# Optimization experiments

Hardware: AMD Instinct MI355X
Metric: run time of the kernel (lower is better)

Reference implementation:

```python
import jax, jax.numpy as jnp
import numpy as np

N = 50000   # nodes
E = 600000  # edges
HID = 128   # node_hidden_channels
G = 128     # num_edge_gaussians
C = 128     # num_node_interaction_channels
EPS = 1e-5  # batchnorm eps


def setup_inputs() -> dict:
    key = jax.random.key(0)
    ks = jax.random.split(key, 12)
    s = lambda k, shape, fan_in: jax.random.normal(k, shape, jnp.float32) / np.sqrt(fan_in)
    return {
        "h": jax.random.normal(ks[0], (N, HID), jnp.float32),
        "edge_index": jax.random.randint(ks[1], (2, E), 0, N),
        "edge_weight": jax.random.uniform(ks[2], (E,), jnp.float32),
        "edge_attr": jax.random.normal(ks[3], (E, G), jnp.float32),
        # lin0: HID -> C
        "W0": s(ks[4], (HID, C), HID), "b0": jnp.zeros((C,), jnp.float32),
        # short: G -> 1
        "Wsh": s(ks[5], (G, 1), G), "bsh": jnp.zeros((1,), jnp.float32),
        # CGConv lin_f / lin_s: (2C+1) -> C, rows ordered [x_i; x_j; edge_attr]
        "Wf": s(ks[6], (2 * C + 1, C), 2 * C + 1), "bf": jnp.zeros((C,), jnp.float32),
        "Ws": s(ks[7], (2 * C + 1, C), 2 * C + 1), "bs": jnp.zeros((C,), jnp.float32),
        # BatchNorm1d affine params
        "gamma": jnp.ones((C,), jnp.float32), "beta": jnp.zeros((C,), jnp.float32),
    }


def reference(h, edge_index, edge_weight, edge_attr, W0, b0, Wsh, bsh, Wf, bf, Ws, bs, gamma, beta):
    src = edge_index[0]  # j (source)
    dst = edge_index[1]  # i (target / aggregation index)

    out = jax.nn.softplus(h @ W0 + b0)                    # [N, C]
    e = jax.nn.softplus(edge_attr @ Wsh + bsh)            # [E, 1]

    # CGConv: z = [x_i, x_j, e]; msg = sigmoid(lin_f(z)) * softplus(lin_s(z))
    # Split the linears so node parts are computed once per node, not per edge.
    pi_f = out @ Wf[:C]          # x_i part  [N, C]
    pj_f = out @ Wf[C:2 * C]     # x_j part  [N, C]
    pi_s = out @ Ws[:C]
    pj_s = out @ Ws[C:2 * C]
    ef = e @ Wf[2 * C:]          # edge part [E, C]
    es = e @ Ws[2 * C:]

    gate = jax.nn.sigmoid(pi_f[dst] + pj_f[src] + ef + bf)   # [E, C]
    core = jax.nn.softplus(pi_s[dst] + pj_s[src] + es + bs)  # [E, C]
    aggr = jax.ops.segment_sum(gate * core, dst, num_segments=N)  # [N, C]

    # BatchNorm1d (training-mode batch statistics) + residual inside CGConv
    mean = jnp.mean(aggr, axis=0)
    var = jnp.var(aggr, axis=0)
    bn = (aggr - mean) * jax.lax.rsqrt(var + EPS) * gamma + beta
    conv_out = bn + out

    # _Interactions: out = out + conv(out)
    return out + conv_out
```

## Files before the change

### kernel.cpp

```cpp
#include <hip/hip_runtime.h>
#include <cmath>

#define NN 50000
#define EE 600000

#define LOG2E 1.44269504088896340736f
#define LN2F  0.69314718055994530942f

__device__ __forceinline__ float fast_exp2(float x) { return __builtin_amdgcn_exp2f(x); }
__device__ __forceinline__ float fast_log2(float x) { return __builtin_amdgcn_logf(x); }
__device__ __forceinline__ float fast_rcp(float x)  { return __builtin_amdgcn_rcpf(x); }

__device__ __forceinline__ float softplus_fast(float x) {
  float x2 = x * LOG2E;
  return LN2F * (fmaxf(x2, 0.f) + fast_log2(1.f + fast_exp2(-fabsf(x2))));
}

__global__ __launch_bounds__(256) void zero_kernel(int* __restrict__ deg,
                                                   float* __restrict__ stats_f) {
  int i = blockIdx.x * 256 + threadIdx.x;
  if (i < NN) deg[i] = 0;
  if (i < 512) stats_f[i] = 0.f;
}

__global__ __launch_bounds__(256) void gemm128_act(const float* __restrict__ A,
                                                   const float* __restrict__ B,
                                                   const float* __restrict__ bias,
                                                   float* __restrict__ Cmat,
                                                   int nrows) {
  __shared__ float Ash[64][68];
  __shared__ float Bsh[64][128];
  const int tid = threadIdx.x;
  const int row0 = blockIdx.x * 64;
  const int tx = tid & 15, ty = tid >> 4;
  const int r0 = ty * 4, c0 = tx * 4;

  float acc[4][8];
#pragma unroll
  for (int r = 0; r < 4; ++r)
#pragma unroll
    for (int j = 0; j < 8; ++j) acc[r][j] = 0.f;

  for (int kb = 0; kb < 2; ++kb) {
    for (int i = tid; i < 64 * 16; i += 256) {
      int r = i >> 4, k4 = i & 15;
      int gr = row0 + r; if (gr >= nrows) gr = nrows - 1;
      float4 v = ((const float4*)(A + (size_t)gr * 128 + kb * 64))[k4];
      *(float4*)&Ash[r][k4 * 4] = v;
    }
    for (int i = tid; i < 64 * 32; i += 256) {
      int k = i >> 5, c4 = i & 31;
      float4 v = ((const float4*)(B + (size_t)(kb * 64 + k) * 128))[c4];
      *(float4*)&Bsh[k][c4 * 4] = v;
    }
    __syncthreads();
#pragma unroll 4
    for (int k = 0; k < 64; ++k) {
      float aa[4] = {Ash[r0 + 0][k], Ash[r0 + 1][k], Ash[r0 + 2][k], Ash[r0 + 3][k]};
      float4 b0 = *(const float4*)&Bsh[k][c0];
      float4 b1 = *(const float4*)&Bsh[k][c0 + 64];
      float bb[8] = {b0.x, b0.y, b0.z, b0.w, b1.x, b1.y, b1.z, b1.w};
#pragma unroll
      for (int r = 0; r < 4; ++r)
#pragma unroll
        for (int j = 0; j < 8; ++j) acc[r][j] = fmaf(aa[r], bb[j], acc[r][j]);
    }
    __syncthreads();
  }

  float bv[8];
#pragma unroll
  for (int j = 0; j < 8; ++j) bv[j] = bias[j < 4 ? c0 + j : c0 + 60 + j];
#pragma unroll
  for (int r = 0; r < 4; ++r) {
    int gr = row0 + r0 + r;
    if (gr < nrows) {
      float tmp[8];
#pragma unroll
      for (int j = 0; j < 8; ++j) tmp[j] = softplus_fast(acc[r][j] + bv[j]);
      *(float4*)(Cmat + (size_t)gr * 128 + c0) = make_float4(tmp[0], tmp[1], tmp[2], tmp[3]);
      *(float4*)(Cmat + (size_t)gr * 128 + c0 + 64) = make_float4(tmp[4], tmp[5], tmp[6], tmp[7]);
    }
  }
}

__global__ __launch_bounds__(256) void gemm128_p4(const float* __restrict__ A,
                                                  const float* __restrict__ Wf,
                                                  const float* __restrict__ Ws,
                                                  const float* __restrict__ bf,
                                                  const float* __restrict__ bs,
                                                  float* __restrict__ Pif,
                                                  float* __restrict__ Pjf,
                                                  float* __restrict__ Pis,
                                                  float* __restrict__ Pjs,
                                                  int nrows) {
  __shared__ float Ash[64][68];
  __shared__ float Bsh[64][128];
  const int tid = threadIdx.x;
  const int row0 = blockIdx.x * 64;
  const int which = blockIdx.y;

  const float* B;  const float* bias;  float* Cmat;
  if (which == 0)      { B = Wf;             bias = bf;      Cmat = Pif; }
  else if (which == 1) { B = Wf + 128 * 128; bias = nullptr; Cmat = Pjf; }
  else if (which == 2) { B = Ws;             bias = bs;      Cmat = Pis; }
  else                 { B = Ws + 128 * 128; bias = nullptr; Cmat = Pjs; }

  const int tx = tid & 15, ty = tid >> 4;
  const int r0 = ty * 4, c0 = tx * 4;

  float acc[4][8];
#pragma unroll
  for (int r = 0; r < 4; ++r)
#pragma unroll
    for (int j = 0; j < 8; ++j) acc[r][j] = 0.f;

  for (int kb = 0; kb < 2; ++kb) {
    for (int i = tid; i < 64 * 16; i += 256) {
      int r = i >> 4, k4 = i & 15;
      int gr = row0 + r; if (gr >= nrows) gr = nrows - 1;
      float4 v = ((const float4*)(A + (size_t)gr * 128 + kb * 64))[k4];
      *(float4*)&Ash[r][k4 * 4] = v;
    }
    for (int i = tid; i < 64 * 32; i += 256) {
      int k = i >> 5, c4 = i & 31;
      float4 v = ((const float4*)(B + (size_t)(kb * 64 + k) * 128))[c4];
      *(float4*)&Bsh[k][c4 * 4] = v;
    }
    __syncthreads();
#pragma unroll 4
    for (int k = 0; k < 64; ++k) {
      float aa[4] = {Ash[r0 + 0][k], Ash[r0 + 1][k], Ash[r0 + 2][k], Ash[r0 + 3][k]};
      float4 b0 = *(const float4*)&Bsh[k][c0];
      float4 b1 = *(const float4*)&Bsh[k][c0 + 64];
      float bb[8] = {b0.x, b0.y, b0.z, b0.w, b1.x, b1.y, b1.z, b1.w};
#pragma unroll
      for (int r = 0; r < 4; ++r)
#pragma unroll
        for (int j = 0; j < 8; ++j) acc[r][j] = fmaf(aa[r], bb[j], acc[r][j]);
    }
    __syncthreads();
  }

  float bv[8];
#pragma unroll
  for (int j = 0; j < 8; ++j)
    bv[j] = bias ? bias[j < 4 ? c0 + j : c0 + 60 + j] : 0.f;
#pragma unroll
  for (int r = 0; r < 4; ++r) {
    int gr = row0 + r0 + r;
    if (gr < nrows) {
      float tmp[8];
#pragma unroll
      for (int j = 0; j < 8; ++j) tmp[j] = (acc[r][j] + bv[j]) * LOG2E;
      *(float4*)(Cmat + (size_t)gr * 128 + c0) = make_float4(tmp[0], tmp[1], tmp[2], tmp[3]);
      *(float4*)(Cmat + (size_t)gr * 128 + c0 + 64) = make_float4(tmp[4], tmp[5], tmp[6], tmp[7]);
    }
  }
}

__global__ __launch_bounds__(256) void edge_e_kernel(const float* __restrict__ edge_attr,
                                                     const float* __restrict__ Wsh,
                                                     const float* __restrict__ bsh,
                                                     float* __restrict__ ebuf) {
  __shared__ float wsh[128];
  int tid = threadIdx.x;
  if (tid < 128) wsh[tid] = Wsh[tid];
  __syncthreads();
  int wave = tid >> 6, lane = tid & 63;
  int sub = lane >> 4, l16 = lane & 15;
  int edge = (blockIdx.x * 4 + wave) * 4 + sub;
  const float4* row = (const float4*)(edge_attr + (size_t)edge * 128);
  float4 v0 = row[l16], v1 = row[l16 + 16];
  float4 w0 = *(const float4*)&wsh[l16 * 4];
  float4 w1 = *(const float4*)&wsh[64 + l16 * 4];
  float p = v0.x * w0.x + v0.y * w0.y + v0.z * w0.z + v0.w * w0.w +
            v1.x * w1.x + v1.y * w1.y + v1.z * w1.z + v1.w * w1.w;
  p += __shfl_xor(p, 1);
  p += __shfl_xor(p, 2);
  p += __shfl_xor(p, 4);
  p += __shfl_xor(p, 8);
  if (l16 == 0) ebuf[edge] = softplus_fast(p + bsh[0]);
}

__global__ __launch_bounds__(256) void hist_kernel(const int* __restrict__ eidx,
                                                   int* __restrict__ deg) {
  int e = blockIdx.x * 256 + threadIdx.x;
  if (e < EE) atomicAdd(&deg[eidx[EE + e]], 1);
}

__global__ __launch_bounds__(1024) void scan_kernel(const int* __restrict__ deg,
                                                    int* __restrict__ rowptr,
                                                    int* __restrict__ cur) {
  __shared__ int wscan[16];
  __shared__ int chunk_total_sh;
  int tid = threadIdx.x;
  int wid = tid >> 6, lane = tid & 63;
  int running = 0;
  for (int base = 0; base < NN; base += 4096) {
    int i0 = base + tid * 4;
    int4 v = make_int4(0, 0, 0, 0);
    if (i0 + 3 < NN) {
      v = *(const int4*)(deg + i0);
    } else {
      if (i0 < NN)     v.x = deg[i0];
      if (i0 + 1 < NN) v.y = deg[i0 + 1];
      if (i0 + 2 < NN) v.z = deg[i0 + 2];
      if (i0 + 3 < NN) v.w = deg[i0 + 3];
    }
    int t0 = v.x, t1 = t0 + v.y, t2 = t1 + v.z, t3 = t2 + v.w;
    int s = t3;
#pragma unroll
    for (int off = 1; off < 64; off <<= 1) {
      int t = __shfl_up(s, off);
      if (lane >= off) s += t;
    }
    if (lane == 63) wscan[wid] = s;
    __syncthreads();
    if (wid == 0 && lane < 16) {
      int w = wscan[lane];
#pragma unroll
      for (int off = 1; off < 16; off <<= 1) {
        int t = __shfl_up(w, off);
        if (lane >= off) w += t;
      }
      wscan[lane] = w;
      if (lane == 15) chunk_total_sh = w;
    }
    __syncthreads();
    int wexcl = (wid == 0) ? 0 : wscan[wid - 1];
    int texcl = running + wexcl + (s - t3);
    int4 r = make_int4(texcl, texcl + t0, texcl + t1, texcl + t2);
    if (i0 + 3 < NN) {
      *(int4*)(rowptr + i0) = r;
      *(int4*)(cur + i0) = r;
    } else {
      if (i0 < NN)     { rowptr[i0] = r.x;     cur[i0] = r.x; }
      if (i0 + 1 < NN) { rowptr[i0 + 1] = r.y; cur[i0 + 1] = r.y; }
      if (i0 + 2 < NN) { rowptr[i0 + 2] = r.z; cur[i0 + 2] = r.z; }
      if (i0 + 3 < NN) { rowptr[i0 + 3] = r.w; cur[i0 + 3] = r.w; }
    }
    running += chunk_total_sh;
    __syncthreads();
  }
  if (tid == 0) rowptr[NN] = EE;
}

__global__ __launch_bounds__(256) void scatter_kernel(const int* __restrict__ eidx,
                                                      const float* __restrict__ ebuf,
                                                      int* __restrict__ cur,
                                                      int* __restrict__ srcs,
                                                      float* __restrict__ evals) {
  int e = blockIdx.x * 256 + threadIdx.x;
  if (e < EE) {
    int dst = eidx[EE + e];
    int pos = atomicAdd(&cur[dst], 1);
    srcs[pos] = eidx[e];
    evals[pos] = ebuf[e];
  }
}

__global__ __launch_bounds__(256) void aggregate_kernel(const int* __restrict__ rowptr,
                                                        const int* __restrict__ srcs,
                                                        const float* __restrict__ evals,
                                                        float* __restrict__ pifagg,
                                                        const float* __restrict__ Pjf,
                                                        const float* __restrict__ Pis,
                                                        const float* __restrict__ Pjs,
                                                        const float* __restrict__ Wf_e,
                                                        const float* __restrict__ Ws_e) {
  __shared__ float wfe[128], wse[128];
  int tid = threadIdx.x;
  if (tid < 128) wfe[tid] = Wf_e[tid] * LOG2E;
  else wse[tid - 128] = Ws_e[tid - 128] * LOG2E;
  __syncthreads();
  int slot = tid >> 5, lane = tid & 31;
  int node = blockIdx.x * 8 + slot;
  float4 fi = ((const float4*)(pifagg + (size_t)node * 128))[lane];
  float4 si = ((const float4*)(Pis + (size_t)node * 128))[lane];
  float4 wf4 = *(const float4*)&wfe[lane * 4];
  float4 ws4 = *(const float4*)&wse[lane * 4];
  float4 acc = make_float4(0.f, 0.f, 0.f, 0.f);

  int beg = rowptr[node], end = rowptr[node + 1];
  if (beg < end) {
    int src = srcs[beg];
    float eV = evals[beg];
    float4 fj = ((const float4*)(Pjf + (size_t)src * 128))[lane];
    float4 sj = ((const float4*)(Pjs + (size_t)src * 128))[lane];
    int sN = 0; float eN = 0.f;
    if (beg + 1 < end) { sN = srcs[beg + 1]; eN = evals[beg + 1]; }
    for (int k = beg; ; ) {
      bool more = (k + 1 < end);
      float4 fjn, sjn;
      if (more) {
        fjn = ((const float4*)(Pjf + (size_t)sN * 128))[lane];
        sjn = ((const float4*)(Pjs + (size_t)sN * 128))[lane];
      }
      int sNN = 0; float eNN = 0.f;
      if (k + 2 < end) { sNN = srcs[k + 2]; eNN = evals[k + 2]; }
      {
        float a2, b2, g, sp;
        a2 = fmaf(eV, wf4.x, fi.x) + fj.x;
        g  = fast_rcp(1.f + fast_exp2(-a2));
        b2 = fmaf(eV, ws4.x, si.x) + sj.x;
        sp = fmaxf(b2, 0.f) + fast_log2(1.f + fast_exp2(-fabsf(b2)));
        acc.x = fmaf(g, sp, acc.x);
        a2 = fmaf(eV, wf4.y, fi.y) + fj.y;
        g  = fast_rcp(1.f + fast_exp2(-a2));
        b2 = fmaf(eV, ws4.y, si.y) + sj.y;
        sp = fmaxf(b2, 0.f) + fast_log2(1.f + fast_exp2(-fabsf(b2)));
        acc.y = fmaf(g, sp, acc.y);
        a2 = fmaf(eV, wf4.z, fi.z) + fj.z;
        g  = fast_rcp(1.f + fast_exp2(-a2));
        b2 = fmaf(eV, ws4.z, si.z) + sj.z;
        sp = fmaxf(b2, 0.f) + fast_log2(1.f + fast_exp2(-fabsf(b2)));
        acc.z = fmaf(g, sp, acc.z);
        a2 = fmaf(eV, wf4.w, fi.w) + fj.w;
        g  = fast_rcp(1.f + fast_exp2(-a2));
        b2 = fmaf(eV, ws4.w, si.w) + sj.w;
        sp = fmaxf(b2, 0.f) + fast_log2(1.f + fast_exp2(-fabsf(b2)));
        acc.w = fmaf(g, sp, acc.w);
      }
      if (!more) break;
      fj = fjn; sj = sjn; eV = eN; sN = sNN; eN = eNN; ++k;
    }
  }
  acc.x *= LN2F; acc.y *= LN2F; acc.z *= LN2F; acc.w *= LN2F;
  ((float4*)(pifagg + (size_t)node * 128))[lane] = acc;
}

__global__ __launch_bounds__(256) void stats_kernel(const float* __restrict__ aggr,
                                                    double* __restrict__ dstats) {
  int tid = threadIdx.x;
  int c = tid & 127, half = tid >> 7;
  int rbase = blockIdx.x * 512;
  float s = 0.f, q = 0.f;
  for (int i = 0; i < 256; ++i) {
    int r = rbase + half + i * 2;
    if (r < NN) {
      float v = aggr[(size_t)r * 128 + c];
      s += v;
      q += v * v;
    }
  }
  __shared__ float shs[256], shq[256];
  shs[tid] = s;
  shq[tid] = q;
  __syncthreads();
  if (tid < 128) {
    double ts = (double)shs[tid] + (double)shs[tid + 128];
    double tq = (double)shq[tid] + (double)shq[tid + 128];
    atomicAdd(&dstats[c], ts);
    atomicAdd(&dstats[128 + c], tq);
  }
}

__global__ void bn_params_kernel(const double* __restrict__ dstats,
                                 const float* __restrict__ gamma,
                                 const float* __restrict__ beta,
                                 float* __restrict__ scsh) {
  int c = threadIdx.x;
  double mean = dstats[c] / (double)NN;
  double var = dstats[128 + c] / (double)NN - mean * mean;
  double rs = 1.0 / sqrt(var + 1e-5);
  double sc = (double)gamma[c] * rs;
  scsh[c] = (float)sc;
  scsh[128 + c] = (float)((double)beta[c] - mean * sc);
}

__global__ __launch_bounds__(256) void finalize_kernel(const float* __restrict__ outbuf,
                                                       const float* __restrict__ scsh,
                                                       float* __restrict__ dout) {
  __shared__ float sc[128], sh[128];
  int tid = threadIdx.x;
  if (tid < 128) sc[tid] = scsh[tid];
  else sh[tid - 128] = scsh[tid];
  __syncthreads();
  size_t i = (size_t)blockIdx.x * 256 + tid;
  size_t stride = (size_t)gridDim.x * 256;
  const float4* o4 = (const float4*)outbuf;
  float4* d4 = (float4*)dout;
  const size_t n4 = (size_t)NN * 32;
  for (; i < n4; i += stride) {
    int c4 = (int)(i & 31) * 4;
    float4 a = d4[i], o = o4[i];
    float4 r;
    r.x = 2.f * o.x + a.x * sc[c4 + 0] + sh[c4 + 0];
    r.y = 2.f * o.y + a.y * sc[c4 + 1] + sh[c4 + 1];
    r.z = 2.f * o.z + a.z * sc[c4 + 2] + sh[c4 + 2];
    r.w = 2.f * o.w + a.w * sc[c4 + 3] + sh[c4 + 3];
    d4[i] = r;
  }
}

extern "C" void kernel_launch(void* const* d_in, const int* in_sizes, int n_in,
                              void* d_out, int out_size, void* d_ws, size_t ws_size,
                              hipStream_t stream) {
  const float* h         = (const float*)d_in[0];
  const int*   eidx      = (const int*)d_in[1];
  const float* edge_attr = (const float*)d_in[3];
  const float* W0    = (const float*)d_in[4];
  const float* b0    = (const float*)d_in[5];
  const float* Wsh   = (const float*)d_in[6];
  const float* bsh   = (const float*)d_in[7];
  const float* Wf    = (const float*)d_in[8];
  const float* bf    = (const float*)d_in[9];
  const float* Ws    = (const float*)d_in[10];
  const float* bs    = (const float*)d_in[11];
  const float* gamma = (const float*)d_in[12];
  const float* beta  = (const float*)d_in[13];
  float* dout = (float*)d_out;

  char* ws = (char*)d_ws;
  const size_t NCb = (size_t)NN * 128 * 4;
  float*  outbuf = (float*)ws;
  float*  Pjf    = (float*)(ws + NCb);
  float*  Pis    = (float*)(ws + NCb * 2);
  float*  Pjs    = (float*)(ws + NCb * 3);
  char*   p0     = ws + NCb * 4;
  float*  ebuf   = (float*)p0;                  p0 += (size_t)EE * 4;
  int*    srcs   = (int*)p0;                    p0 += (size_t)EE * 4;
  float*  evals  = (float*)p0;                  p0 += (size_t)EE * 4;
  double* dstats = (double*)p0;                 p0 += 256 * 8;
  float*  scsh   = (float*)p0;                  p0 += 256 * 4;
  int*    deg    = (int*)p0;                    p0 += (size_t)NN * 4;
  int*    rowptr = (int*)p0;                    p0 += (size_t)(NN + 4) * 4;
  int*    cur    = (int*)p0;
  float*  Pif    = dout;

  zero_kernel<<<(NN + 255) / 256, 256, 0, stream>>>(deg, (float*)dstats);

  const int gblocks = (NN + 63) / 64;
  gemm128_act<<<gblocks, 256, 0, stream>>>(h, W0, b0, outbuf, NN);

  gemm128_p4<<<dim3(gblocks, 4), 256, 0, stream>>>(outbuf, Wf, Ws, bf, bs,
                                                   Pif, Pjf, Pis, Pjs, NN);

  edge_e_kernel<<<EE / 16, 256, 0, stream>>>(edge_attr, Wsh, bsh, ebuf);

  hist_kernel<<<(EE + 255) / 256, 256, 0, stream>>>(eidx, deg);
  scan_kernel<<<1, 1024, 0, stream>>>(deg, rowptr, cur);
  scatter_kernel<<<(EE + 255) / 256, 256, 0, stream>>>(eidx, ebuf, cur, srcs, evals);

  aggregate_kernel<<<NN / 8, 256, 0, stream>>>(rowptr, srcs, evals, Pif, Pjf, Pis, Pjs,
                                               Wf + 256 * 128, Ws + 256 * 128);

  stats_kernel<<<(NN + 511) / 512, 256, 0, stream>>>(dout, dstats);
  bn_params_kernel<<<1, 128, 0, stream>>>(dstats, gamma, beta, scsh);
  finalize_kernel<<<2048, 256, 0, stream>>>(outbuf, scsh, dout);
}
```

Before: 823.3 us.

## Store node projections as interleaved fp16, pack edge records, fuse histogram

Node projection matrices are now stored as fp16, with the f and s parts interleaved per node into an own-buffer and a gather-buffer, so each edge gather is one 16-byte load instead of two float4 loads. Source index and edge value are packed into a single int2 record, the degree histogram is folded into the edge_e kernel, and the aggregate loop prefetches two edges ahead. This cuts gather bandwidth and launch count, at the cost of fp16 rounding on the pre-activation inputs.

```diff
diff --git a/kernel.cpp b/kernel.cpp
--- a/kernel.cpp
+++ b/kernel.cpp
@@ -1,4 +1,5 @@
 #include <hip/hip_runtime.h>
+#include <hip/hip_fp16.h>
 #include <cmath>
 
 #define NN 50000
@@ -89,10 +90,8 @@
                                                   const float* __restrict__ Ws,
                                                   const float* __restrict__ bf,
                                                   const float* __restrict__ bs,
-                                                  float* __restrict__ Pif,
-                                                  float* __restrict__ Pjf,
-                                                  float* __restrict__ Pis,
-                                                  float* __restrict__ Pjs,
+                                                  ushort* __restrict__ POwn,
+                                                  ushort* __restrict__ PGat,
                                                   int nrows) {
   __shared__ float Ash[64][68];
   __shared__ float Bsh[64][128];
@@ -100,11 +99,11 @@
   const int row0 = blockIdx.x * 64;
   const int which = blockIdx.y;
 
-  const float* B;  const float* bias;  float* Cmat;
-  if (which == 0)      { B = Wf;             bias = bf;      Cmat = Pif; }
-  else if (which == 1) { B = Wf + 128 * 128; bias = nullptr; Cmat = Pjf; }
-  else if (which == 2) { B = Ws;             bias = bs;      Cmat = Pis; }
-  else                 { B = Ws + 128 * 128; bias = nullptr; Cmat = Pjs; }
+  const float* B;  const float* bias;  ushort* dstbase;  int soff;
+  if (which == 0)      { B = Wf;             bias = bf;      dstbase = POwn; soff = 0; }
+  else if (which == 1) { B = Wf + 128 * 128; bias = nullptr; dstbase = PGat; soff = 0; }
+  else if (which == 2) { B = Ws;             bias = bs;      dstbase = POwn; soff = 4; }
+  else                 { B = Ws + 128 * 128; bias = nullptr; dstbase = PGat; soff = 4; }
 
   const int tx = tid & 15, ty = tid >> 4;
   const int r0 = ty * 4, c0 = tx * 4;
@@ -150,11 +149,17 @@
   for (int r = 0; r < 4; ++r) {
     int gr = row0 + r0 + r;
     if (gr < nrows) {
-      float tmp[8];
-#pragma unroll
-      for (int j = 0; j < 8; ++j) tmp[j] = (acc[r][j] + bv[j]) * LOG2E;
-      *(float4*)(Cmat + (size_t)gr * 128 + c0) = make_float4(tmp[0], tmp[1], tmp[2], tmp[3]);
-      *(float4*)(Cmat + (size_t)gr * 128 + c0 + 64) = make_float4(tmp[4], tmp[5], tmp[6], tmp[7]);
+      ushort4 lo, hi;
+      lo.x = __half_as_ushort(__float2half((acc[r][0] + bv[0]) * LOG2E));
+      lo.y = __half_as_ushort(__float2half((acc[r][1] + bv[1]) * LOG2E));
+      lo.z = __half_as_ushort(__float2half((acc[r][2] + bv[2]) * LOG2E));
+      lo.w = __half_as_ushort(__float2half((acc[r][3] + bv[3]) * LOG2E));
+      hi.x = __half_as_ushort(__float2half((acc[r][4] + bv[4]) * LOG2E));
+      hi.y = __half_as_ushort(__float2half((acc[r][5] + bv[5]) * LOG2E));
+      hi.z = __half_as_ushort(__float2half((acc[r][6] + bv[6]) * LOG2E));
+      hi.w = __half_as_ushort(__float2half((acc[r][7] + bv[7]) * LOG2E));
+      *(ushort4*)(dstbase + (size_t)gr * 256 + tx * 8 + soff) = lo;
+      *(ushort4*)(dstbase + (size_t)gr * 256 + (tx + 16) * 8 + soff) = hi;
     }
   }
 }
@@ -162,11 +167,17 @@
 __global__ __launch_bounds__(256) void edge_e_kernel(const float* __restrict__ edge_attr,
                                                      const float* __restrict__ Wsh,
                                                      const float* __restrict__ bsh,
+                                                     const int* __restrict__ eidx,
+                                                     int* __restrict__ deg,
                                                      float* __restrict__ ebuf) {
   __shared__ float wsh[128];
   int tid = threadIdx.x;
   if (tid < 128) wsh[tid] = Wsh[tid];
   __syncthreads();
+  if (tid < 16) {
+    int e = blockIdx.x * 16 + tid;
+    atomicAdd(&deg[eidx[EE + e]], 1);
+  }
   int wave = tid >> 6, lane = tid & 63;
   int sub = lane >> 4, l16 = lane & 15;
   int edge = (blockIdx.x * 4 + wave) * 4 + sub;
@@ -181,12 +192,6 @@
   p += __shfl_xor(p, 4);
   p += __shfl_xor(p, 8);
   if (l16 == 0) ebuf[edge] = softplus_fast(p + bsh[0]);
-}
-
-__global__ __launch_bounds__(256) void hist_kernel(const int* __restrict__ eidx,
-                                                   int* __restrict__ deg) {
-  int e = blockIdx.x * 256 + threadIdx.x;
-  if (e < EE) atomicAdd(&deg[eidx[EE + e]], 1);
 }
 
 __global__ __launch_bounds__(1024) void scan_kernel(const int* __restrict__ deg,
@@ -249,24 +254,20 @@
 __global__ __launch_bounds__(256) void scatter_kernel(const int* __restrict__ eidx,
                                                       const float* __restrict__ ebuf,
                                                       int* __restrict__ cur,
-                                                      int* __restrict__ srcs,
-                                                      float* __restrict__ evals) {
+                                                      int2* __restrict__ edges) {
   int e = blockIdx.x * 256 + threadIdx.x;
   if (e < EE) {
     int dst = eidx[EE + e];
     int pos = atomicAdd(&cur[dst], 1);
-    srcs[pos] = eidx[e];
-    evals[pos] = ebuf[e];
+    edges[pos] = make_int2(eidx[e], __float_as_int(ebuf[e]));
   }
 }
 
 __global__ __launch_bounds__(256) void aggregate_kernel(const int* __restrict__ rowptr,
-                                                        const int* __restrict__ srcs,
-                                                        const float* __restrict__ evals,
-                                                        float* __restrict__ pifagg,
-                                                        const float* __restrict__ Pjf,
-                                                        const float* __restrict__ Pis,
-                                                        const float* __restrict__ Pjs,
+                                                        const int2* __restrict__ edges,
+                                                        const ushort* __restrict__ POwn,
+                                                        const ushort* __restrict__ PGat,
+                                                        float* __restrict__ aggr,
                                                         const float* __restrict__ Wf_e,
                                                         const float* __restrict__ Ws_e) {
   __shared__ float wfe[128], wse[128];
@@ -276,58 +277,58 @@
   __syncthreads();
   int slot = tid >> 5, lane = tid & 31;
   int node = blockIdx.x * 8 + slot;
-  float4 fi = ((const float4*)(pifagg + (size_t)node * 128))[lane];
-  float4 si = ((const float4*)(Pis + (size_t)node * 128))[lane];
+  const uint4* ownrow = (const uint4*)(POwn + (size_t)node * 256);
+  uint4 o = ownrow[lane];
+  float2 fi01 = __half22float2(*(const __half2*)&o.x);
+  float2 fi23 = __half22float2(*(const __half2*)&o.y);
+  float2 si01 = __half22float2(*(const __half2*)&o.z);
+  float2 si23 = __half22float2(*(const __half2*)&o.w);
   float4 wf4 = *(const float4*)&wfe[lane * 4];
   float4 ws4 = *(const float4*)&wse[lane * 4];
   float4 acc = make_float4(0.f, 0.f, 0.f, 0.f);
 
   int beg = rowptr[node], end = rowptr[node + 1];
   if (beg < end) {
-    int src = srcs[beg];
-    float eV = evals[beg];
-    float4 fj = ((const float4*)(Pjf + (size_t)src * 128))[lane];
-    float4 sj = ((const float4*)(Pjs + (size_t)src * 128))[lane];
-    int sN = 0; float eN = 0.f;
-    if (beg + 1 < end) { sN = srcs[beg + 1]; eN = evals[beg + 1]; }
-    for (int k = beg; ; ) {
-      bool more = (k + 1 < end);
-      float4 fjn, sjn;
-      if (more) {
-        fjn = ((const float4*)(Pjf + (size_t)sN * 128))[lane];
-        sjn = ((const float4*)(Pjs + (size_t)sN * 128))[lane];
-      }
-      int sNN = 0; float eNN = 0.f;
-      if (k + 2 < end) { sNN = srcs[k + 2]; eNN = evals[k + 2]; }
-      {
-        float a2, b2, g, sp;
-        a2 = fmaf(eV, wf4.x, fi.x) + fj.x;
-        g  = fast_rcp(1.f + fast_exp2(-a2));
-        b2 = fmaf(eV, ws4.x, si.x) + sj.x;
-        sp = fmaxf(b2, 0.f) + fast_log2(1.f + fast_exp2(-fabsf(b2)));
-        acc.x = fmaf(g, sp, acc.x);
-        a2 = fmaf(eV, wf4.y, fi.y) + fj.y;
-        g  = fast_rcp(1.f + fast_exp2(-a2));
-        b2 = fmaf(eV, ws4.y, si.y) + sj.y;
-        sp = fmaxf(b2, 0.f) + fast_log2(1.f + fast_exp2(-fabsf(b2)));
-        acc.y = fmaf(g, sp, acc.y);
-        a2 = fmaf(eV, wf4.z, fi.z) + fj.z;
-        g  = fast_rcp(1.f + fast_exp2(-a2));
-        b2 = fmaf(eV, ws4.z, si.z) + sj.z;
-        sp = fmaxf(b2, 0.f) + fast_log2(1.f + fast_exp2(-fabsf(b2)));
-        acc.z = fmaf(g, sp, acc.z);
-        a2 = fmaf(eV, wf4.w, fi.w) + fj.w;
-        g  = fast_rcp(1.f + fast_exp2(-a2));
-        b2 = fmaf(eV, ws4.w, si.w) + sj.w;
-        sp = fmaxf(b2, 0.f) + fast_log2(1.f + fast_exp2(-fabsf(b2)));
-        acc.w = fmaf(g, sp, acc.w);
-      }
-      if (!more) break;
-      fj = fjn; sj = sjn; eV = eN; sN = sNN; eN = eNN; ++k;
+    const uint4* gat = (const uint4*)PGat;
+    int2 eA = edges[beg];
+    int2 eB = edges[min(beg + 1, end - 1)];
+    uint4 gA = gat[(size_t)eA.x * 32 + lane];
+    uint4 gB = gat[(size_t)eB.x * 32 + lane];
+    for (int k = beg; k < end; ++k) {
+      int2 eC = edges[min(k + 2, end - 1)];
+      uint4 gC = gat[(size_t)eC.x * 32 + lane];
+      float eV = __int_as_float(eA.y);
+      float2 fj01 = __half22float2(*(const __half2*)&gA.x);
+      float2 fj23 = __half22float2(*(const __half2*)&gA.y);
+      float2 sj01 = __half22float2(*(const __half2*)&gA.z);
+      float2 sj23 = __half22float2(*(const __half2*)&gA.w);
+      float a2, b2, g, sp;
+      a2 = fmaf(eV, wf4.x, fi01.x) + fj01.x;
+      g  = fast_rcp(1.f + fast_exp2(-a2));
+      b2 = fmaf(eV, ws4.x, si01.x) + sj01.x;
+      sp = fmaxf(b2, 0.f) + fast_log2(1.f + fast_exp2(-fabsf(b2)));
+      acc.x = fmaf(g, sp, acc.x);
+      a2 = fmaf(eV, wf4.y, fi01.y) + fj01.y;
+      g  = fast_rcp(1.f + fast_exp2(-a2));
+      b2 = fmaf(eV, ws4.y, si01.y) + sj01.y;
+      sp = fmaxf(b2, 0.f) + fast_log2(1.f + fast_exp2(-fabsf(b2)));
+      acc.y = fmaf(g, sp, acc.y);
+      a2 = fmaf(eV, wf4.z, fi23.x) + fj23.x;
+      g  = fast_rcp(1.f + fast_exp2(-a2));
+      b2 = fmaf(eV, ws4.z, si23.x) + sj23.x;
+      sp = fmaxf(b2, 0.f) + fast_log2(1.f + fast_exp2(-fabsf(b2)));
+      acc.z = fmaf(g, sp, acc.z);
+      a2 = fmaf(eV, wf4.w, fi23.y) + fj23.y;
+      g  = fast_rcp(1.f + fast_exp2(-a2));
+      b2 = fmaf(eV, ws4.w, si23.y) + sj23.y;
+      sp = fmaxf(b2, 0.f) + fast_log2(1.f + fast_exp2(-fabsf(b2)));
+      acc.w = fmaf(g, sp, acc.w);
+      eA = eB; gA = gB;
+      eB = eC; gB = gC;
     }
   }
   acc.x *= LN2F; acc.y *= LN2F; acc.z *= LN2F; acc.w *= LN2F;
-  ((float4*)(pifagg + (size_t)node * 128))[lane] = acc;
+  ((float4*)(aggr + (size_t)node * 128))[lane] = acc;
 }
 
 __global__ __launch_bounds__(256) void stats_kernel(const float* __restrict__ aggr,
@@ -414,20 +415,18 @@
 
   char* ws = (char*)d_ws;
   const size_t NCb = (size_t)NN * 128 * 4;
+  const size_t NHb = (size_t)NN * 256 * 2;
   float*  outbuf = (float*)ws;
-  float*  Pjf    = (float*)(ws + NCb);
-  float*  Pis    = (float*)(ws + NCb * 2);
-  float*  Pjs    = (float*)(ws + NCb * 3);
-  char*   p0     = ws + NCb * 4;
+  ushort* POwn   = (ushort*)(ws + NCb);
+  ushort* PGat   = (ushort*)(ws + NCb + NHb);
+  char*   p0     = ws + NCb + NHb * 2;
   float*  ebuf   = (float*)p0;                  p0 += (size_t)EE * 4;
-  int*    srcs   = (int*)p0;                    p0 += (size_t)EE * 4;
-  float*  evals  = (float*)p0;                  p0 += (size_t)EE * 4;
+  int2*   edges  = (int2*)p0;                   p0 += (size_t)EE * 8;
   double* dstats = (double*)p0;                 p0 += 256 * 8;
   float*  scsh   = (float*)p0;                  p0 += 256 * 4;
   int*    deg    = (int*)p0;                    p0 += (size_t)NN * 4;
   int*    rowptr = (int*)p0;                    p0 += (size_t)(NN + 4) * 4;
   int*    cur    = (int*)p0;
-  float*  Pif    = dout;
 
   zero_kernel<<<(NN + 255) / 256, 256, 0, stream>>>(deg, (float*)dstats);
 
@@ -435,15 +434,14 @@
   gemm128_act<<<gblocks, 256, 0, stream>>>(h, W0, b0, outbuf, NN);
 
   gemm128_p4<<<dim3(gblocks, 4), 256, 0, stream>>>(outbuf, Wf, Ws, bf, bs,
-                                                   Pif, Pjf, Pis, Pjs, NN);
-
-  edge_e_kernel<<<EE / 16, 256, 0, stream>>>(edge_attr, Wsh, bsh, ebuf);
-
-  hist_kernel<<<(EE + 255) / 256, 256, 0, stream>>>(eidx, deg);
+                                                   POwn, PGat, NN);
+
+  edge_e_kernel<<<EE / 16, 256, 0, stream>>>(edge_attr, Wsh, bsh, eidx, deg, ebuf);
+
   scan_kernel<<<1, 1024, 0, stream>>>(deg, rowptr, cur);
-  scatter_kernel<<<(EE + 255) / 256, 256, 0, stream>>>(eidx, ebuf, cur, srcs, evals);
-
-  aggregate_kernel<<<NN / 8, 256, 0, stream>>>(rowptr, srcs, evals, Pif, Pjf, Pis, Pjs,
+  scatter_kernel<<<(EE + 255) / 256, 256, 0, stream>>>(eidx, ebuf, cur, edges);
+
+  aggregate_kernel<<<NN / 8, 256, 0, stream>>>(rowptr, edges, POwn, PGat, dout,
                                                Wf + 256 * 128, Ws + 256 * 128);
 
   stats_kernel<<<(NN + 511) / 512, 256, 0, stream>>>(dout, dstats);
```

Measured after the change: 770.6 us. 6.4% less time.
